# Optimization experiments

Measured on AMD Instinct MI355X. Metric: run time of the kernel, lower is better.

Reference implementation:

```python
import jax, jax.numpy as jnp
import numpy as np
from jax import lax

B, C_IN, N, C_OUT, K = 8, 64, 4096, 64, 20
EPS = 1e-5
NEG_SLOPE = 0.2


def setup_inputs() -> dict:
    key = jax.random.key(0)
    k1, k2, k3, k4, k5, k6 = jax.random.split(key, 6)
    x = jax.random.normal(k1, (B, C_IN, N), dtype=jnp.float32)
    # Conv2d(2*C_in, C_out, kernel_size=1, bias=False) -> weight (C_out, 2*C_in)
    W = jax.random.normal(k2, (C_OUT, 2 * C_IN), dtype=jnp.float32) * (1.0 / np.sqrt(2 * C_IN))
    gamma = jax.random.normal(k3, (C_OUT,), dtype=jnp.float32) * 0.1 + 1.0
    beta = jax.random.normal(k4, (C_OUT,), dtype=jnp.float32) * 0.1
    running_mean = jax.random.normal(k5, (C_OUT,), dtype=jnp.float32) * 0.1
    running_var = jax.random.uniform(k6, (C_OUT,), dtype=jnp.float32, minval=0.5, maxval=1.5)
    return {"x": x, "W": W, "gamma": gamma, "beta": beta,
            "running_mean": running_mean, "running_var": running_var}


def reference(x, W, gamma, beta, running_mean, running_var):
    # x: (B, C, N)
    # ---- KNN graph: pairwise squared distances, top-k nearest (includes self) ----
    xx = jnp.sum(x * x, axis=1)                       # (B, N)
    inner = jnp.einsum('bcn,bcm->bnm', x, x)          # (B, N, N)
    d2 = xx[:, :, None] - 2.0 * inner + xx[:, None, :]  # (B, N, N)
    _, idx = lax.top_k(-d2, K)                        # (B, N, K) int32 indices

    # ---- gather neighbor features ----
    xt = jnp.transpose(x, (0, 2, 1))                  # (B, N, C)
    neighbors = jax.vmap(lambda feats, i: feats[i])(xt, idx)  # (B, N, K, C)
    central = xt[:, :, None, :]                       # (B, N, 1, C) broadcast over K

    # ---- edge features: [x_i, x_j - x_i] -> (B, N, K, 2C) ----
    edge = jnp.concatenate(
        [jnp.broadcast_to(central, (B, N, K, C_IN)), neighbors - central], axis=-1)

    # ---- 1x1 conv (pointwise matmul) + BatchNorm (eval mode) + LeakyReLU ----
    h = jnp.einsum('bnkc,oc->bnko', edge, W)          # (B, N, K, C_out)
    inv_std = lax.rsqrt(running_var + EPS)
    h = (h - running_mean) * (inv_std * gamma) + beta
    h = jnp.where(h >= 0, h, NEG_SLOPE * h)           # LeakyReLU(0.2)

    # ---- max over k neighbors, return (B, C_out, N) ----
    out = jnp.max(h, axis=2)                          # (B, N, C_out)
    return jnp.transpose(out, (0, 2, 1))
```

## Files before the change

### kernel.cpp

```cpp
#include <hip/hip_runtime.h>

#define NB 8
#define NC 64
#define NN 4096
#define NO 64
#define KK 20
#define EPSV 1e-5f
#define SLOPE 0.2f

typedef __attribute__((ext_vector_type(8))) short short8x;
typedef __attribute__((ext_vector_type(4))) float float4x;


__device__ __forceinline__ unsigned short bfh(float f) {
  unsigned u = __float_as_uint(f);
  unsigned r = u + 0x7FFFu + ((u >> 16) & 1u);
  return (unsigned short)(r >> 16);
}

__device__ __forceinline__ unsigned flipf(float f) {
  unsigned u = __float_as_uint(f);
  return u ^ ((unsigned)((int)u >> 31) | 0x80000000u);
}

__global__ void k0_wprep(const float* __restrict__ W,
                         float* __restrict__ wa, float* __restrict__ wb) {
  int t = threadIdx.x;
  for (int i = t; i < NC * NO; i += 256) {
    int o = i & 63, c = i >> 6;
    float w1 = W[o * 128 + c];
    float w2 = W[o * 128 + 64 + c];
    wa[i] = w1 - w2;
    wb[i] = w2;
  }
}

__global__ __launch_bounds__(256) void k1_feat(const float* __restrict__ x,
    const float* __restrict__ waT, const float* __restrict__ wbT,
    float* __restrict__ y1, float* __restrict__ y2, float* __restrict__ xxg,
    unsigned short* __restrict__ xThi, unsigned short* __restrict__ xTmid,
    unsigned short* __restrict__ xTlo) {
  __shared__ __align__(16) float xs[NC * 68];
  __shared__ __align__(16) float wa[NC * NO];
  __shared__ __align__(16) float wb[NC * NO];
  int t = threadIdx.x;
  int b = blockIdx.x >> 6;
  int gr0 = (blockIdx.x & 63) << 6;
  const float* xb = x + (size_t)b * NC * NN;
  #pragma unroll
  for (int k = 0; k < 4; ++k) {
    int i4 = t + k * 256;
    int c = i4 >> 4, col4 = (i4 & 15) << 2;
    *(float4*)&xs[c * 68 + col4] = *(const float4*)&xb[(size_t)c * NN + gr0 + col4];
    *(float4*)&wa[c * 64 + col4] = *(const float4*)&waT[c * 64 + col4];
    *(float4*)&wb[c * 64 + col4] = *(const float4*)&wbT[c * 64 + col4];
  }
  __syncthreads();
  if (t < 64) {
    float s = 0.f;
    #pragma unroll
    for (int c = 0; c < NC; ++c) { float v = xs[c * 68 + t]; s = fmaf(v, v, s); }
    xxg[b * NN + gr0 + t] = s;
  }
  int o = t & 63, w = t >> 6;
  for (int j = 0; j < 16; ++j) {
    int n = j * 4 + w;
    float a1 = 0.f, a2 = 0.f;
    #pragma unroll
    for (int c = 0; c < NC; ++c) {
      float xv = xs[c * 68 + n];
      a1 = fmaf(wa[c * 64 + o], xv, a1);
      a2 = fmaf(wb[c * 64 + o], xv, a2);
    }
    size_t base = ((size_t)b * NN + gr0 + n) * NO + o;
    y1[base] = a1;
    y2[base] = a2;
  }
  int n2 = t >> 2, c0 = (t & 3) << 4;
  short8x vh[2], vm[2], vl[2];
  #pragma unroll
  for (int i = 0; i < 16; ++i) {
    float v = xs[(c0 + i) * 68 + n2];
    unsigned short h = bfh(v);
    float hf = __uint_as_float((unsigned)h << 16);
    float r1 = v - hf;
    unsigned short md = bfh(r1);
    float mf = __uint_as_float((unsigned)md << 16);
    unsigned short lo = bfh(r1 - mf);
    vh[i >> 3][i & 7] = (short)h;
    vm[i >> 3][i & 7] = (short)md;
    vl[i >> 3][i & 7] = (short)lo;
  }
  size_t tb = ((size_t)(b * NN + gr0 + n2)) * 64 + c0;
  *(short8x*)&xThi[tb] = vh[0];  *(short8x*)&xThi[tb + 8] = vh[1];
  *(short8x*)&xTmid[tb] = vm[0]; *(short8x*)&xTmid[tb + 8] = vm[1];
  *(short8x*)&xTlo[tb] = vl[0];  *(short8x*)&xTlo[tb + 8] = vl[1];
}

__global__ __launch_bounds__(256, 3) void k2_topk(
    const unsigned short* __restrict__ xThi, const unsigned short* __restrict__ xTmid,
    const unsigned short* __restrict__ xTlo, const float* __restrict__ xxg,
    unsigned* __restrict__ keyuG, unsigned short* __restrict__ idxG) {
  __shared__ __align__(16) unsigned short Rb[3 * 4096];
  __shared__ __align__(16) unsigned candU[64 * 68];
  __shared__ __align__(16) float xxs[64];
  __shared__ __align__(16) unsigned cutq[256];

  int t = threadIdx.x;
  int blk = blockIdx.x;
  int b = blk >> 7;
  int rem = blk & 127;
  int rg = rem >> 1, half = rem & 1;
  int gr0 = rg << 6;
  int gc0 = half << 11;
  int w = t >> 6;
  int lm = t & 15;
  int quad = (t >> 4) & 3;
  int orow = t & 63, oq = t >> 6;

  size_t abase = ((size_t)(b * NN + gr0 + 16 * w + lm)) * 64;
  short8x Ah[2], Am[2], Al[2];
  #pragma unroll
  for (int ks = 0; ks < 2; ++ks) {
    int co = ks * 32 + quad * 8;
    Ah[ks] = *(const short8x*)&xThi[abase + co];
    Am[ks] = *(const short8x*)&xTmid[abase + co];
    Al[ks] = *(const short8x*)&xTlo[abase + co];
  }
  cutq[t] = 0xFFFFFFFFu;

  unsigned long long lst[KK];
  #pragma unroll
  for (int j = 0; j < KK; ++j) lst[j] = ~0ull;

  size_t bbase = (size_t)(b * NN) * 64;
  unsigned* wrow = &candU[(16 * w + quad * 4) * 68 + lm];
  const unsigned* crow = &candU[orow * 68 + oq * 16];

  for (int mt = 0; mt < 32; ++mt) {
    int gm0 = gc0 + (mt << 6);
    __syncthreads();
    #pragma unroll
    for (int lvl = 0; lvl < 3; ++lvl) {
      const unsigned short* src = (lvl == 0) ? xThi : (lvl == 1) ? xTmid : xTlo;
      unsigned short* dst = Rb + lvl * 4096;
      #pragma unroll
      for (int p = 0; p < 2; ++p) {
        int idx = p * 256 + t;
        int n = idx >> 3, o = idx & 7;
        *(short8x*)&dst[n * 64 + ((o + n) & 7) * 8] =
            *(const short8x*)&src[bbase + (size_t)(gm0 + n) * 64 + o * 8];
      }
    }
    if (t < 16) *(float4*)&xxs[t * 4] = *(const float4*)&xxg[b * NN + gm0 + t * 4];
    __syncthreads();

    float4x acc[4];
    #pragma unroll
    for (int j = 0; j < 4; ++j) acc[j] = (float4x){0.f, 0.f, 0.f, 0.f};

    const unsigned short* RbH = Rb;
    const unsigned short* RbM = Rb + 4096;
    const unsigned short* RbL = Rb + 8192;
    #pragma unroll
    for (int ks = 0; ks < 2; ++ks) {
      #pragma unroll
      for (int j = 0; j < 4; ++j) {
        int n = 16 * j + lm;
        int off = n * 64 + ((ks * 4 + quad + n) & 7) * 8;
        short8x bh = *(const short8x*)&RbH[off];
        short8x bm = *(const short8x*)&RbM[off];
        short8x bl = *(const short8x*)&RbL[off];
        acc[j] = __builtin_amdgcn_mfma_f32_16x16x32_bf16(Am[ks], bm, acc[j], 0, 0, 0);
        acc[j] = __builtin_amdgcn_mfma_f32_16x16x32_bf16(Ah[ks], bl, acc[j], 0, 0, 0);
        acc[j] = __builtin_amdgcn_mfma_f32_16x16x32_bf16(Al[ks], bh, acc[j], 0, 0, 0);
        acc[j] = __builtin_amdgcn_mfma_f32_16x16x32_bf16(Ah[ks], bm, acc[j], 0, 0, 0);
        acc[j] = __builtin_amdgcn_mfma_f32_16x16x32_bf16(Am[ks], bh, acc[j], 0, 0, 0);
        acc[j] = __builtin_amdgcn_mfma_f32_16x16x32_bf16(Ah[ks], bh, acc[j], 0, 0, 0);
      }
    }

    float xq[4];
    #pragma unroll
    for (int j = 0; j < 4; ++j) xq[j] = xxs[16 * j + lm];

    #pragma unroll
    for (int j = 0; j < 4; ++j) {
      #pragma unroll
      for (int q = 0; q < 4; ++q) {
        float key = fmaf(-2.f, acc[j][q], xq[j]);
        wrow[q * 68 + 16 * j] = flipf(key);
      }
    }
    __syncthreads();

    uint4 cq = *(const uint4*)&cutq[orow * 4];
    unsigned thr = min(min(cq.x, cq.y), min(cq.z, cq.w));
    unsigned own19 = (unsigned)(lst[KK - 1] >> 12);
    thr = min(thr, own19);
    uint4 v0 = *(const uint4*)&crow[0];
    uint4 v1 = *(const uint4*)&crow[4];
    uint4 v2 = *(const uint4*)&crow[8];
    uint4 v3 = *(const uint4*)&crow[12];
    unsigned mask = 0;
    mask |= (unsigned)(v0.x <= thr) << 0;
    mask |= (unsigned)(v0.y <= thr) << 1;
    mask |= (unsigned)(v0.z <= thr) << 2;
    mask |= (unsigned)(v0.w <= thr) << 3;
    mask |= (unsigned)(v1.x <= thr) << 4;
    mask |= (unsigned)(v1.y <= thr) << 5;
    mask |= (unsigned)(v1.z <= thr) << 6;
    mask |= (unsigned)(v1.w <= thr) << 7;
    mask |= (unsigned)(v2.x <= thr) << 8;
    mask |= (unsigned)(v2.y <= thr) << 9;
    mask |= (unsigned)(v2.z <= thr) << 10;
    mask |= (unsigned)(v2.w <= thr) << 11;
    mask |= (unsigned)(v3.x <= thr) << 12;
    mask |= (unsigned)(v3.y <= thr) << 13;
    mask |= (unsigned)(v3.z <= thr) << 14;
    mask |= (unsigned)(v3.w <= thr) << 15;
    while (mask) {
      int e = __builtin_ctz(mask);
      mask &= mask - 1;
      unsigned ku = crow[e];
      int c = oq * 16 + e;
      unsigned long long p = ((unsigned long long)ku << 12) | (unsigned)(gm0 + c);
      if (p < lst[KK - 1]) {
        #pragma unroll
        for (int j = KK - 1; j >= 1; --j) {
          bool sh = p < lst[j - 1];
          unsigned long long cur = (p < lst[j]) ? p : lst[j];
          lst[j] = sh ? lst[j - 1] : cur;
        }
        if (p < lst[0]) lst[0] = p;
      }
    }
    cutq[orow * 4 + oq] = (unsigned)(lst[KK - 1] >> 12);
  }

  unsigned long long* M = (unsigned long long*)Rb;
  #pragma unroll 1
  for (int ph = 0; ph < 2; ++ph) {
    __syncthreads();
    if ((orow >> 5) == ph) {
      int r5 = orow & 31;
      #pragma unroll
      for (int k = 0; k < KK; ++k) M[r5 * 84 + oq * 21 + k] = lst[k];
      M[r5 * 84 + oq * 21 + KK] = ~0ull;
    }
    __syncthreads();
    if (t < 32) {
      int h0 = 0, h1 = 0, h2 = 0, h3 = 0;
      int rb = t * 84;
      int row = ph * 32 + t;
      size_t base = ((size_t)(b * NN + gr0 + row) * 2 + half) * KK;
      for (int k = 0; k < KK; ++k) {
        unsigned long long v0m = M[rb + h0];
        unsigned long long v1m = M[rb + 21 + h1];
        unsigned long long v2m = M[rb + 42 + h2];
        unsigned long long v3m = M[rb + 63 + h3];
        unsigned long long bv = v0m; int bq = 0;
        if (v1m < bv) { bv = v1m; bq = 1; }
        if (v2m < bv) { bv = v2m; bq = 2; }
        if (v3m < bv) { bv = v3m; bq = 3; }
        keyuG[base + k] = (unsigned)(bv >> 12);
        idxG[base + k] = (unsigned short)(bv & 0xFFFu);
        if (bq == 0) h0++; else if (bq == 1) h1++; else if (bq == 2) h2++; else h3++;
      }
    }
  }
}

__global__ __launch_bounds__(256) void k3_out(const float* __restrict__ y1,
    const float* __restrict__ y2, const unsigned* __restrict__ keyuG,
    const unsigned short* __restrict__ idxG,
    const float* __restrict__ gamma, const float* __restrict__ beta,
    const float* __restrict__ rmean, const float* __restrict__ rvar,
    float* __restrict__ out) {
  __shared__ int sidx[64 * KK];
  __shared__ float ot[64 * 65];
  int t = threadIdx.x;
  int b = blockIdx.x >> 6;
  int gr0 = (blockIdx.x & 63) << 6;
  if (t < 64) {
    size_t base0 = ((size_t)(b * NN + gr0 + t) * 2) * KK;
    size_t base1 = base0 + KK;
    int h0 = 0, h1 = 0;
    for (int k = 0; k < KK; ++k) {
      int a0 = h0 < KK ? h0 : KK - 1;
      int a1 = h1 < KK ? h1 : KK - 1;
      unsigned k0v = keyuG[base0 + a0]; unsigned i0 = idxG[base0 + a0];
      unsigned k1v = keyuG[base1 + a1]; unsigned i1 = idxG[base1 + a1];
      bool take0 = (h1 >= KK) ||
                   ((h0 < KK) && (k0v < k1v || (k0v == k1v && i0 < i1)));
      sidx[t * KK + k] = take0 ? (int)i0 : (int)i1;
      if (take0) h0++; else h1++;
    }
  }
  int l = t & 63, w = t >> 6;
  float sc = gamma[l] * rsqrtf(rvar[l] + EPSV);
  float tt = fmaf(-rmean[l], sc, beta[l]);
  __syncthreads();
  const float* y2b = y2 + (size_t)b * NN * NO;
  for (int rr = 0; rr < 16; ++rr) {
    int row = w * 16 + rr;
    float v1 = y1[((size_t)b * NN + gr0 + row) * NO + l];
    int mk[KK];
    #pragma unroll
    for (int k = 0; k < KK; ++k) mk[k] = sidx[row * KK + k];
    float vv[KK];
    #pragma unroll
    for (int k = 0; k < KK; ++k) vv[k] = y2b[(size_t)mk[k] * NO + l];
    float best = -3.4e38f;
    #pragma unroll
    for (int k = 0; k < KK; ++k) {
      float v = v1 + vv[k];
      v = fmaf(v, sc, tt);
      v = v >= 0.f ? v : SLOPE * v;
      best = fmaxf(best, v);
    }
    ot[l * 65 + row] = best;
  }
  __syncthreads();
  float* ob = out + (size_t)b * NO * NN;
  for (int i = t; i < 4096; i += 256) {
    int o = i >> 6, n = i & 63;
    ob[(size_t)o * NN + gr0 + n] = ot[o * 65 + n];
  }
}

extern "C" void kernel_launch(void* const* d_in, const int* in_sizes, int n_in,
                              void* d_out, int out_size, void* d_ws, size_t ws_size,
                              hipStream_t stream) {
  const float* x     = (const float*)d_in[0];
  const float* W     = (const float*)d_in[1];
  const float* gamma = (const float*)d_in[2];
  const float* beta  = (const float*)d_in[3];
  const float* rmean = (const float*)d_in[4];
  const float* rvar  = (const float*)d_in[5];
  float* ws  = (float*)d_ws;
  float* y1    = ws;
  float* y2    = ws + 2097152;
  float* xx    = ws + 4194304;
  unsigned* keyu = (unsigned*)(ws + 4227072);
  unsigned short* idxu = (unsigned short*)(ws + 5537792);
  float* wa    = ws + 6193152;
  float* wb    = ws + 6197248;
  unsigned short* xThi  = (unsigned short*)(ws + 6201344);
  unsigned short* xTmid = (unsigned short*)(ws + 7249920);
  unsigned short* xTlo  = (unsigned short*)(ws + 8298496);
  float* out = (float*)d_out;

  hipLaunchKernelGGL(k0_wprep, dim3(1),    dim3(256), 0, stream, W, wa, wb);
  hipLaunchKernelGGL(k1_feat,  dim3(512),  dim3(256), 0, stream, x, wa, wb, y1, y2, xx,
                     xThi, xTmid, xTlo);
  hipLaunchKernelGGL(k2_topk,  dim3(1024), dim3(256), 0, stream, xThi, xTmid, xTlo,
                     xx, keyu, idxu);
  hipLaunchKernelGGL(k3_out,   dim3(512),  dim3(256), 0, stream, y1, y2, keyu, idxu,
                     gamma, beta, rmean, rvar, out);
}
```

Measured before the change: 384.9 us.

## Swap MFMA operands so each lane holds row candidates directly, drop LDS transpose

The MFMA operand order is swapped so the accumulator layout gives each lane four candidate columns of its own query row. The lane can then filter and insert into its top-k list straight from registers, with no round trip through shared memory. This removes the candU staging buffer, the cutq threshold exchange and one block barrier per tile. The threshold is now shared across the four lanes of a row with cross-lane shuffles, and it is computed before the tile rather than from other lanes' updated lists, so filtering may be somewhat looser.

```diff
diff --git a/kernel.cpp b/kernel.cpp
--- a/kernel.cpp
+++ b/kernel.cpp
@@ -21,6 +21,10 @@
 __device__ __forceinline__ unsigned flipf(float f) {
   unsigned u = __float_as_uint(f);
   return u ^ ((unsigned)((int)u >> 31) | 0x80000000u);
+}
+
+__device__ __forceinline__ unsigned unflipu(unsigned v) {
+  return v ^ (0x80000000u | (unsigned)((int)(~v) >> 31));
 }
 
 __global__ void k0_wprep(const float* __restrict__ W,
@@ -102,9 +106,7 @@
     const unsigned short* __restrict__ xTlo, const float* __restrict__ xxg,
     unsigned* __restrict__ keyuG, unsigned short* __restrict__ idxG) {
   __shared__ __align__(16) unsigned short Rb[3 * 4096];
-  __shared__ __align__(16) unsigned candU[64 * 68];
   __shared__ __align__(16) float xxs[64];
-  __shared__ __align__(16) unsigned cutq[256];
 
   int t = threadIdx.x;
   int blk = blockIdx.x;
@@ -116,7 +118,6 @@
   int w = t >> 6;
   int lm = t & 15;
   int quad = (t >> 4) & 3;
-  int orow = t & 63, oq = t >> 6;
 
   size_t abase = ((size_t)(b * NN + gr0 + 16 * w + lm)) * 64;
   short8x Ah[2], Am[2], Al[2];
@@ -127,15 +128,12 @@
     Am[ks] = *(const short8x*)&xTmid[abase + co];
     Al[ks] = *(const short8x*)&xTlo[abase + co];
   }
-  cutq[t] = 0xFFFFFFFFu;
 
   unsigned long long lst[KK];
   #pragma unroll
   for (int j = 0; j < KK; ++j) lst[j] = ~0ull;
 
   size_t bbase = (size_t)(b * NN) * 64;
-  unsigned* wrow = &candU[(16 * w + quad * 4) * 68 + lm];
-  const unsigned* crow = &candU[orow * 68 + oq * 16];
 
   for (int mt = 0; mt < 32; ++mt) {
     int gm0 = gc0 + (mt << 6);
@@ -171,73 +169,61 @@
         short8x bh = *(const short8x*)&RbH[off];
         short8x bm = *(const short8x*)&RbM[off];
         short8x bl = *(const short8x*)&RbL[off];
-        acc[j] = __builtin_amdgcn_mfma_f32_16x16x32_bf16(Am[ks], bm, acc[j], 0, 0, 0);
-        acc[j] = __builtin_amdgcn_mfma_f32_16x16x32_bf16(Ah[ks], bl, acc[j], 0, 0, 0);
-        acc[j] = __builtin_amdgcn_mfma_f32_16x16x32_bf16(Al[ks], bh, acc[j], 0, 0, 0);
-        acc[j] = __builtin_amdgcn_mfma_f32_16x16x32_bf16(Ah[ks], bm, acc[j], 0, 0, 0);
-        acc[j] = __builtin_amdgcn_mfma_f32_16x16x32_bf16(Am[ks], bh, acc[j], 0, 0, 0);
-        acc[j] = __builtin_amdgcn_mfma_f32_16x16x32_bf16(Ah[ks], bh, acc[j], 0, 0, 0);
-      }
-    }
-
-    float xq[4];
-    #pragma unroll
-    for (int j = 0; j < 4; ++j) xq[j] = xxs[16 * j + lm];
-
+        acc[j] = __builtin_amdgcn_mfma_f32_16x16x32_bf16(bm, Am[ks], acc[j], 0, 0, 0);
+        acc[j] = __builtin_amdgcn_mfma_f32_16x16x32_bf16(bl, Ah[ks], acc[j], 0, 0, 0);
+        acc[j] = __builtin_amdgcn_mfma_f32_16x16x32_bf16(bh, Al[ks], acc[j], 0, 0, 0);
+        acc[j] = __builtin_amdgcn_mfma_f32_16x16x32_bf16(bm, Ah[ks], acc[j], 0, 0, 0);
+        acc[j] = __builtin_amdgcn_mfma_f32_16x16x32_bf16(bh, Am[ks], acc[j], 0, 0, 0);
+        acc[j] = __builtin_amdgcn_mfma_f32_16x16x32_bf16(bh, Ah[ks], acc[j], 0, 0, 0);
+      }
+    }
+
+    unsigned own19u = (unsigned)(lst[KK - 1] >> 12);
+    own19u = min(own19u, 0xFF7FFFFFu);
+    float thr = __uint_as_float(unflipu(own19u));
+    thr = fminf(thr, __shfl_xor(thr, 16));
+    thr = fminf(thr, __shfl_xor(thr, 32));
+
+    float key[16];
+    unsigned mask = 0;
     #pragma unroll
     for (int j = 0; j < 4; ++j) {
+      float4 xq = *(const float4*)&xxs[16 * j + 4 * quad];
+      const float* xqp = (const float*)&xq;
       #pragma unroll
       for (int q = 0; q < 4; ++q) {
-        float key = fmaf(-2.f, acc[j][q], xq[j]);
-        wrow[q * 68 + 16 * j] = flipf(key);
-      }
-    }
-    __syncthreads();
-
-    uint4 cq = *(const uint4*)&cutq[orow * 4];
-    unsigned thr = min(min(cq.x, cq.y), min(cq.z, cq.w));
-    unsigned own19 = (unsigned)(lst[KK - 1] >> 12);
-    thr = min(thr, own19);
-    uint4 v0 = *(const uint4*)&crow[0];
-    uint4 v1 = *(const uint4*)&crow[4];
-    uint4 v2 = *(const uint4*)&crow[8];
-    uint4 v3 = *(const uint4*)&crow[12];
-    unsigned mask = 0;
-    mask |= (unsigned)(v0.x <= thr) << 0;
-    mask |= (unsigned)(v0.y <= thr) << 1;
-    mask |= (unsigned)(v0.z <= thr) << 2;
-    mask |= (unsigned)(v0.w <= thr) << 3;
-    mask |= (unsigned)(v1.x <= thr) << 4;
-    mask |= (unsigned)(v1.y <= thr) << 5;
-    mask |= (unsigned)(v1.z <= thr) << 6;
-    mask |= (unsigned)(v1.w <= thr) << 7;
-    mask |= (unsigned)(v2.x <= thr) << 8;
-    mask |= (unsigned)(v2.y <= thr) << 9;
-    mask |= (unsigned)(v2.z <= thr) << 10;
-    mask |= (unsigned)(v2.w <= thr) << 11;
-    mask |= (unsigned)(v3.x <= thr) << 12;
-    mask |= (unsigned)(v3.y <= thr) << 13;
-    mask |= (unsigned)(v3.z <= thr) << 14;
-    mask |= (unsigned)(v3.w <= thr) << 15;
-    while (mask) {
-      int e = __builtin_ctz(mask);
-      mask &= mask - 1;
-      unsigned ku = crow[e];
-      int c = oq * 16 + e;
-      unsigned long long p = ((unsigned long long)ku << 12) | (unsigned)(gm0 + c);
-      if (p < lst[KK - 1]) {
-        #pragma unroll
-        for (int j = KK - 1; j >= 1; --j) {
-          bool sh = p < lst[j - 1];
-          unsigned long long cur = (p < lst[j]) ? p : lst[j];
-          lst[j] = sh ? lst[j - 1] : cur;
+        float kv = fmaf(-2.f, acc[j][q], xqp[q]);
+        key[4 * j + q] = kv;
+        mask |= (unsigned)(kv <= thr) << (4 * j + q);
+      }
+    }
+
+    #pragma unroll
+    for (int j = 0; j < 4; ++j) {
+      unsigned sm = (mask >> (4 * j)) & 0xFu;
+      while (sm) {
+        int e = __builtin_ctz(sm);
+        sm &= sm - 1;
+        float k01 = (e & 2) ? key[4 * j + 3] : key[4 * j + 1];
+        float k00 = (e & 2) ? key[4 * j + 2] : key[4 * j + 0];
+        float kv = (e & 1) ? k01 : k00;
+        unsigned ku = flipf(kv);
+        int c = 16 * j + (quad << 2) + e;
+        unsigned long long p = ((unsigned long long)ku << 12) | (unsigned)(gm0 + c);
+        if (p < lst[KK - 1]) {
+          #pragma unroll
+          for (int jj = KK - 1; jj >= 1; --jj) {
+            bool sh = p < lst[jj - 1];
+            unsigned long long cur = (p < lst[jj]) ? p : lst[jj];
+            lst[jj] = sh ? lst[jj - 1] : cur;
+          }
+          if (p < lst[0]) lst[0] = p;
         }
-        if (p < lst[0]) lst[0] = p;
-      }
-    }
-    cutq[orow * 4 + oq] = (unsigned)(lst[KK - 1] >> 12);
-  }
-
+      }
+    }
+  }
+
+  int orow = 16 * w + lm, oq = quad;
   unsigned long long* M = (unsigned long long*)Rb;
   #pragma unroll 1
   for (int ph = 0; ph < 2; ++ph) {
```

Measured after the change: 476.9 us. 1.24x slower.
